# Optimization experiments

Measured on AMD Instinct MI355X. Metric: run time of the kernel, lower is better.

## Reference

```python
import jax, jax.numpy as jnp
import numpy as np

B = 16384
I = 1024  # inputs_size
H = 1024  # hidden_size


def _linear_params(key, fan_in, fan_out):
    # torch nn.Linear default init: U(-1/sqrt(fan_in), 1/sqrt(fan_in))
    kw, kb = jax.random.split(key)
    bound = 1.0 / np.sqrt(fan_in)
    W = jax.random.uniform(kw, (fan_out, fan_in), jnp.float32, -bound, bound)
    b = jax.random.uniform(kb, (fan_out,), jnp.float32, -bound, bound)
    return W, b


def setup_inputs() -> dict:
    key = jax.random.key(0)
    ks = jax.random.split(key, 8)
    inp = {
        "input": jax.random.normal(ks[0], (B, I), jnp.float32),
        "hidden": jax.random.normal(ks[1], (B, H), jnp.float32),
    }
    names = ["r_i", "r_h", "z_i", "z_h", "n_i", "n_h"]
    fan_ins = [I, H, I, H, I, H]
    for name, fi, k in zip(names, fan_ins, ks[2:]):
        W, b = _linear_params(k, fi, H)
        inp[f"W_{name}"] = W
        inp[f"b_{name}"] = b
    return inp


def reference(input, hidden,
              W_r_i, b_r_i, W_r_h, b_r_h,
              W_z_i, b_z_i, W_z_h, b_z_h,
              W_n_i, b_n_i, W_n_h, b_n_h):
    # Faithful to the original (including its bug: z uses r_layer_h(hidden)).
    r_h = hidden @ W_r_h.T + b_r_h  # reused by both r and z gates
    r = jax.nn.sigmoid(input @ W_r_i.T + b_r_i + r_h)
    z = jax.nn.sigmoid(input @ W_z_i.T + b_z_i + r_h)
    n = jnp.tanh(input @ W_n_i.T + b_n_i + r * (hidden @ W_n_h.T + b_n_h))
    next_hidden = (1.0 - z) * n + z * hidden
    return (next_hidden, next_hidden)
```

## Files before the change

kernel.cpp:

```cpp
#include <hip/hip_runtime.h>


#define BM 128
#define BN 64
#define BK 32
#define LDW 40

typedef __attribute__((ext_vector_type(8))) short  bf16x8;
typedef __attribute__((ext_vector_type(4))) float  f32x4;

__device__ __forceinline__ unsigned short f2bf(float f) {
    union { float f; unsigned u; } v; v.f = f;
    unsigned r = v.u + 0x7FFFu + ((v.u >> 16) & 1u);
    return (unsigned short)(r >> 16);
}

__device__ __forceinline__ void stage4(unsigned short* dst, const float4 v) {
    ushort4 u;
    u.x = f2bf(v.x); u.y = f2bf(v.y); u.z = f2bf(v.z); u.w = f2bf(v.w);
    *reinterpret_cast<ushort4*>(dst) = u;
}

__global__ __launch_bounds__(256, 2) void gru_fused(
    const float* __restrict__ input, const float* __restrict__ hidden,
    const float* __restrict__ W_ri, const float* __restrict__ b_ri,
    const float* __restrict__ W_rh, const float* __restrict__ b_rh,
    const float* __restrict__ W_zi, const float* __restrict__ b_zi,
    const float* __restrict__ W_ni, const float* __restrict__ b_ni,
    const float* __restrict__ W_nh, const float* __restrict__ b_nh,
    float* __restrict__ out)
{
    const int H = 1024, K = 1024;
    const int BH = 16384 * 1024;

    __shared__ __align__(16) unsigned short sIn [BM][LDW];
    __shared__ __align__(16) unsigned short sHid[BM][LDW];
    __shared__ __align__(16) unsigned short sW[5][BN][LDW];

    const int tid  = threadIdx.x;
    const int wave = tid >> 6;
    const int lane = tid & 63;
    const int quad = lane >> 4;
    const int l16  = lane & 15;

    const int row0 = blockIdx.y * BM;
    const int col0 = blockIdx.x * BN;

    const float* Wg[5] = { W_ri, W_rh, W_zi, W_ni, W_nh };

    f32x4 acc[5][2][4];
    #pragma unroll
    for (int g = 0; g < 5; ++g)
        #pragma unroll
        for (int mi = 0; mi < 2; ++mi)
            #pragma unroll
            for (int ni = 0; ni < 4; ++ni)
                acc[g][mi][ni] = (f32x4){0.f, 0.f, 0.f, 0.f};

    const int sr = tid >> 3;
    const int sc = (tid & 7) << 2;

    for (int k0 = 0; k0 < K; k0 += BK) {
        __syncthreads();
        #pragma unroll
        for (int p = 0; p < 4; ++p) {
            const int r = p * 32 + sr;
            const float4 vi = *reinterpret_cast<const float4*>(&input [(row0 + r) * K + k0 + sc]);
            const float4 vh = *reinterpret_cast<const float4*>(&hidden[(row0 + r) * K + k0 + sc]);
            stage4(&sIn [r][sc], vi);
            stage4(&sHid[r][sc], vh);
        }
        #pragma unroll
        for (int g = 0; g < 5; ++g) {
            #pragma unroll
            for (int p = 0; p < 2; ++p) {
                const int idx = p * 256 + tid;
                const int r = idx >> 3;
                const int c = (idx & 7) << 2;
                const float4 v = *reinterpret_cast<const float4*>(&Wg[g][(col0 + r) * K + k0 + c]);
                stage4(&sW[g][r][c], v);
            }
        }
        __syncthreads();

        bf16x8 aIn[2], aHid[2];
        #pragma unroll
        for (int mi = 0; mi < 2; ++mi) {
            const int r = wave * 32 + mi * 16 + l16;
            aIn [mi] = *reinterpret_cast<const bf16x8*>(&sIn [r][quad * 8]);
            aHid[mi] = *reinterpret_cast<const bf16x8*>(&sHid[r][quad * 8]);
        }
        #pragma unroll
        for (int g = 0; g < 5; ++g) {
            #pragma unroll
            for (int ni = 0; ni < 4; ++ni) {
                const bf16x8 b = *reinterpret_cast<const bf16x8*>(&sW[g][ni * 16 + l16][quad * 8]);
                #pragma unroll
                for (int mi = 0; mi < 2; ++mi) {
                    const bf16x8 a = (g == 1 || g == 4) ? aHid[mi] : aIn[mi];
                    acc[g][mi][ni] = __builtin_amdgcn_mfma_f32_16x16x32_bf16(a, b, acc[g][mi][ni], 0, 0, 0);
                }
            }
        }
    }

    #pragma unroll
    for (int ni = 0; ni < 4; ++ni) {
        const int gcol = col0 + ni * 16 + l16;
        const float bri = b_ri[gcol], brh = b_rh[gcol], bzi = b_zi[gcol];
        const float bni = b_ni[gcol], bnh = b_nh[gcol];
        #pragma unroll
        for (int mi = 0; mi < 2; ++mi) {
            #pragma unroll
            for (int r4 = 0; r4 < 4; ++r4) {
                const int grow = row0 + wave * 32 + mi * 16 + quad * 4 + r4;
                const float g_ri = acc[0][mi][ni][r4];
                const float g_rh = acc[1][mi][ni][r4];
                const float g_zi = acc[2][mi][ni][r4];
                const float g_ni = acc[3][mi][ni][r4];
                const float g_nh = acc[4][mi][ni][r4];
                const float rh = g_rh + brh;
                const float rr = 1.f / (1.f + __expf(-(g_ri + bri + rh)));
                const float zz = 1.f / (1.f + __expf(-(g_zi + bzi + rh)));
                const float nn = tanhf(g_ni + bni + rr * (g_nh + bnh));
                const float h  = hidden[grow * H + gcol];
                const float o  = (1.f - zz) * nn + zz * h;
                out[grow * H + gcol]      = o;
                out[BH + grow * H + gcol] = o;
            }
        }
    }
}

extern "C" void kernel_launch(void* const* d_in, const int* in_sizes, int n_in,
                              void* d_out, int out_size, void* d_ws, size_t ws_size,
                              hipStream_t stream) {
    const float* input = (const float*)d_in[0];
    const float* hidden = (const float*)d_in[1];
    const float* W_ri = (const float*)d_in[2];
    const float* b_ri = (const float*)d_in[3];
    const float* W_rh = (const float*)d_in[4];
    const float* b_rh = (const float*)d_in[5];
    const float* W_zi = (const float*)d_in[6];
    const float* b_zi = (const float*)d_in[7];
    const float* W_ni = (const float*)d_in[10];
    const float* b_ni = (const float*)d_in[11];
    const float* W_nh = (const float*)d_in[12];
    const float* b_nh = (const float*)d_in[13];
    float* out = (float*)d_out;

    dim3 grid(1024 / BN, 16384 / BM);
    gru_fused<<<grid, 256, 0, stream>>>(input, hidden,
                                        W_ri, b_ri, W_rh, b_rh,
                                        W_zi, b_zi, W_ni, b_ni,
                                        W_nh, b_nh, out);
}
```

Measured before the change: 602.3 us.

## Pre-convert operands to bf16 in workspace and stage tiles via direct global-to-LDS loads

Adds a separate pass that converts input, hidden and the five weight matrices to bf16 in the workspace once per call. The GEMM kernel then copies bf16 tiles straight into LDS with global_load_lds instead of loading fp32, converting in registers and storing. This halves the bytes read inside the main loop, which re-reads operands across many blocks, and removes the per-tile conversion work. The cost is an extra pass over about 70 MB of data, and the LDS tile is now unpadded (stride 64 bytes), which may cause bank conflicts on the MFMA operand reads.

```diff
diff --git a/kernel.cpp b/kernel.cpp
--- a/kernel.cpp
+++ b/kernel.cpp
@@ -4,10 +4,10 @@
 #define BM 128
 #define BN 64
 #define BK 32
-#define LDW 40
 
-typedef __attribute__((ext_vector_type(8))) short  bf16x8;
-typedef __attribute__((ext_vector_type(4))) float  f32x4;
+typedef __attribute__((ext_vector_type(8))) short          bf16x8;
+typedef __attribute__((ext_vector_type(8))) unsigned short u16x8;
+typedef __attribute__((ext_vector_type(4))) float          f32x4;
 
 __device__ __forceinline__ unsigned short f2bf(float f) {
     union { float f; unsigned u; } v; v.f = f;
@@ -15,27 +15,51 @@
     return (unsigned short)(r >> 16);
 }
 
-__device__ __forceinline__ void stage4(unsigned short* dst, const float4 v) {
-    ushort4 u;
-    u.x = f2bf(v.x); u.y = f2bf(v.y); u.z = f2bf(v.z); u.w = f2bf(v.w);
-    *reinterpret_cast<ushort4*>(dst) = u;
+__global__ __launch_bounds__(256) void convert_bf16(
+    const float* __restrict__ in0, const float* __restrict__ in1,
+    const float* __restrict__ w0, const float* __restrict__ w1,
+    const float* __restrict__ w2, const float* __restrict__ w3,
+    const float* __restrict__ w4, unsigned short* __restrict__ ws)
+{
+    const long long e = ((long long)blockIdx.x * 256 + threadIdx.x) * 8;
+    const float* src;
+    if (e < 16777216LL) {
+        src = in0 + e;
+    } else if (e < 33554432LL) {
+        src = in1 + (e - 16777216LL);
+    } else {
+        const long long t = e - 33554432LL;
+        const int g = (int)(t >> 20);
+        const long long within = t & 1048575LL;
+        const float* w = (g == 0) ? w0 : (g == 1) ? w1 : (g == 2) ? w2 : (g == 3) ? w3 : w4;
+        src = w + within;
+    }
+    const float4 a = *reinterpret_cast<const float4*>(src);
+    const float4 b = *reinterpret_cast<const float4*>(src + 4);
+    u16x8 o;
+    o[0] = f2bf(a.x); o[1] = f2bf(a.y); o[2] = f2bf(a.z); o[3] = f2bf(a.w);
+    o[4] = f2bf(b.x); o[5] = f2bf(b.y); o[6] = f2bf(b.z); o[7] = f2bf(b.w);
+    *reinterpret_cast<u16x8*>(ws + e) = o;
+}
+
+__device__ __forceinline__ void async16(const void* g, void* l) {
+    __builtin_amdgcn_global_load_lds(
+        (const __attribute__((address_space(1))) unsigned int*)g,
+        (__attribute__((address_space(3))) unsigned int*)l, 16, 0, 0);
 }
 
 __global__ __launch_bounds__(256, 2) void gru_fused(
-    const float* __restrict__ input, const float* __restrict__ hidden,
-    const float* __restrict__ W_ri, const float* __restrict__ b_ri,
-    const float* __restrict__ W_rh, const float* __restrict__ b_rh,
-    const float* __restrict__ W_zi, const float* __restrict__ b_zi,
-    const float* __restrict__ W_ni, const float* __restrict__ b_ni,
-    const float* __restrict__ W_nh, const float* __restrict__ b_nh,
+    const unsigned short* __restrict__ bf,
+    const float* __restrict__ hidden,
+    const float* __restrict__ b_ri, const float* __restrict__ b_rh,
+    const float* __restrict__ b_zi, const float* __restrict__ b_ni,
+    const float* __restrict__ b_nh,
     float* __restrict__ out)
 {
     const int H = 1024, K = 1024;
     const int BH = 16384 * 1024;
 
-    __shared__ __align__(16) unsigned short sIn [BM][LDW];
-    __shared__ __align__(16) unsigned short sHid[BM][LDW];
-    __shared__ __align__(16) unsigned short sW[5][BN][LDW];
+    __shared__ __align__(16) unsigned char sBuf[36864];
 
     const int tid  = threadIdx.x;
     const int wave = tid >> 6;
@@ -46,7 +70,30 @@
     const int row0 = blockIdx.y * BM;
     const int col0 = blockIdx.x * BN;
 
-    const float* Wg[5] = { W_ri, W_rh, W_zi, W_ni, W_nh };
+    const unsigned short* inB  = bf;
+    const unsigned short* hidB = bf + 16777216;
+    const unsigned short* wB   = bf + 33554432;
+
+    const unsigned short* srcbase[9];
+    int ldsoff[9];
+    #pragma unroll
+    for (int j = 0; j < 9; ++j) {
+        const int s = (j * 4 + wave) * 64 + lane;
+        ldsoff[j] = s * 16;
+        if (s < 512) {
+            const int r = s >> 2;
+            srcbase[j] = inB + (long long)(row0 + r) * K + (s & 3) * 8;
+        } else if (s < 1024) {
+            const int r = (s - 512) >> 2;
+            srcbase[j] = hidB + (long long)(row0 + r) * K + (s & 3) * 8;
+        } else {
+            const int t = s - 1024;
+            const int g = t >> 8;
+            const int tt = t & 255;
+            const int n = tt >> 2;
+            srcbase[j] = wB + (long long)g * 1048576 + (long long)(col0 + n) * K + (tt & 3) * 8;
+        }
+    }
 
     f32x4 acc[5][2][4];
     #pragma unroll
@@ -57,44 +104,27 @@
             for (int ni = 0; ni < 4; ++ni)
                 acc[g][mi][ni] = (f32x4){0.f, 0.f, 0.f, 0.f};
 
-    const int sr = tid >> 3;
-    const int sc = (tid & 7) << 2;
-
     for (int k0 = 0; k0 < K; k0 += BK) {
         __syncthreads();
         #pragma unroll
-        for (int p = 0; p < 4; ++p) {
-            const int r = p * 32 + sr;
-            const float4 vi = *reinterpret_cast<const float4*>(&input [(row0 + r) * K + k0 + sc]);
-            const float4 vh = *reinterpret_cast<const float4*>(&hidden[(row0 + r) * K + k0 + sc]);
-            stage4(&sIn [r][sc], vi);
-            stage4(&sHid[r][sc], vh);
-        }
-        #pragma unroll
-        for (int g = 0; g < 5; ++g) {
-            #pragma unroll
-            for (int p = 0; p < 2; ++p) {
-                const int idx = p * 256 + tid;
-                const int r = idx >> 3;
-                const int c = (idx & 7) << 2;
-                const float4 v = *reinterpret_cast<const float4*>(&Wg[g][(col0 + r) * K + k0 + c]);
-                stage4(&sW[g][r][c], v);
-            }
-        }
+        for (int j = 0; j < 9; ++j)
+            async16(srcbase[j] + k0, sBuf + ldsoff[j]);
         __syncthreads();
 
         bf16x8 aIn[2], aHid[2];
         #pragma unroll
         for (int mi = 0; mi < 2; ++mi) {
             const int r = wave * 32 + mi * 16 + l16;
-            aIn [mi] = *reinterpret_cast<const bf16x8*>(&sIn [r][quad * 8]);
-            aHid[mi] = *reinterpret_cast<const bf16x8*>(&sHid[r][quad * 8]);
+            aIn [mi] = *reinterpret_cast<const bf16x8*>(&sBuf[r * 64 + quad * 16]);
+            aHid[mi] = *reinterpret_cast<const bf16x8*>(&sBuf[8192 + r * 64 + quad * 16]);
         }
         #pragma unroll
         for (int g = 0; g < 5; ++g) {
             #pragma unroll
             for (int ni = 0; ni < 4; ++ni) {
-                const bf16x8 b = *reinterpret_cast<const bf16x8*>(&sW[g][ni * 16 + l16][quad * 8]);
+                const int n = ni * 16 + l16;
+                const bf16x8 b = *reinterpret_cast<const bf16x8*>(
+                    &sBuf[16384 + g * 4096 + n * 64 + quad * 16]);
                 #pragma unroll
                 for (int mi = 0; mi < 2; ++mi) {
                     const bf16x8 a = (g == 1 || g == 4) ? aHid[mi] : aIn[mi];
@@ -123,10 +153,10 @@
                 const float rr = 1.f / (1.f + __expf(-(g_ri + bri + rh)));
                 const float zz = 1.f / (1.f + __expf(-(g_zi + bzi + rh)));
                 const float nn = tanhf(g_ni + bni + rr * (g_nh + bnh));
-                const float h  = hidden[grow * H + gcol];
+                const float h  = hidden[(long long)grow * H + gcol];
                 const float o  = (1.f - zz) * nn + zz * h;
-                out[grow * H + gcol]      = o;
-                out[BH + grow * H + gcol] = o;
+                out[(long long)grow * H + gcol]      = o;
+                out[BH + (long long)grow * H + gcol] = o;
             }
         }
     }
@@ -135,7 +165,7 @@
 extern "C" void kernel_launch(void* const* d_in, const int* in_sizes, int n_in,
                               void* d_out, int out_size, void* d_ws, size_t ws_size,
                               hipStream_t stream) {
-    const float* input = (const float*)d_in[0];
+    const float* input  = (const float*)d_in[0];
     const float* hidden = (const float*)d_in[1];
     const float* W_ri = (const float*)d_in[2];
     const float* b_ri = (const float*)d_in[3];
@@ -148,10 +178,10 @@
     const float* W_nh = (const float*)d_in[12];
     const float* b_nh = (const float*)d_in[13];
     float* out = (float*)d_out;
+    unsigned short* ws = (unsigned short*)d_ws;
+
+    convert_bf16<<<18944, 256, 0, stream>>>(input, hidden, W_ri, W_rh, W_zi, W_ni, W_nh, ws);
 
     dim3 grid(1024 / BN, 16384 / BM);
-    gru_fused<<<grid, 256, 0, stream>>>(input, hidden,
-                                        W_ri, b_ri, W_rh, b_rh,
-                                        W_zi, b_zi, W_ni, b_ni,
-                                        W_nh, b_nh, out);
+    gru_fused<<<grid, 256, 0, stream>>>(ws, hidden, b_ri, b_rh, b_zi, b_ni, b_nh, out);
 }
```

New measurement: 504.6 us. -16.2%, faster.
